# Kernel optimization log

Hardware: AMD Instinct MI355X
Metric: run time of the kernel (lower is better)

## Reference

```python
import jax, jax.numpy as jnp
import numpy as np

B, T, DIN, DH, DE, C = 32, 256, 768, 512, 25, 9


def _xavier(k, shape):
    lim = float(np.sqrt(6.0 / (shape[0] + shape[1])))
    return jax.random.uniform(k, shape, jnp.float32, -lim, lim)


def _unif(k, shape, s):
    return jax.random.uniform(k, shape, jnp.float32, -s, s)


def setup_inputs() -> dict:
    key = jax.random.key(0)
    ks = jax.random.split(key, 14)
    s = 1.0 / float(np.sqrt(DH))
    return {
        "X": jax.random.normal(ks[0], (B, T, DIN), jnp.float32),
        "pad": _xavier(ks[1], (1, DIN)),
        "label_emb": _xavier(ks[2], (C + 1, DE)),
        "Wih_f": _unif(ks[3], (3 * DH, 3 * DIN), s),
        "Whh_f": _unif(ks[4], (3 * DH, DH), s),
        "bih_f": _unif(ks[5], (3 * DH,), s),
        "bhh_f": _unif(ks[6], (3 * DH,), s),
        "Wih_b": _unif(ks[7], (3 * DH, 3 * DIN), s),
        "Whh_b": _unif(ks[8], (3 * DH, DH), s),
        "bih_b": _unif(ks[9], (3 * DH,), s),
        "bhh_b": _unif(ks[10], (3 * DH,), s),
        "Wc": _unif(ks[11], (C, 2 * DH + DE), 1.0 / float(np.sqrt(2 * DH + DE))),
        "bc": _unif(ks[12], (C,), 1.0 / float(np.sqrt(2 * DH + DE))),
    }


def _gru_dir(x, Wih, Whh, bih, bhh, reverse):
    # x: [B, T, 3*DIN]; torch GRU gate order r, z, n
    def step(h, xt):
        gi = xt @ Wih.T + bih              # [B, 3H]
        gh = h @ Whh.T + bhh               # [B, 3H]
        ir, iz, i_n = jnp.split(gi, 3, axis=1)
        hr, hz, h_n = jnp.split(gh, 3, axis=1)
        r = jax.nn.sigmoid(ir + hr)
        z = jax.nn.sigmoid(iz + hz)
        n = jnp.tanh(i_n + r * h_n)
        h = (1.0 - z) * n + z * h
        return h, h
    h0 = jnp.zeros((x.shape[0], Whh.shape[1]), x.dtype)
    _, ys = jax.lax.scan(step, h0, jnp.swapaxes(x, 0, 1), reverse=reverse)
    return jnp.swapaxes(ys, 0, 1)          # [B, T, H]


def reference(X, pad, label_emb, Wih_f, Whh_f, bih_f, bhh_f, Wih_b, Whh_b, bih_b, bhh_b, Wc, bc):
    b = X.shape[0]
    pad_b = jnp.broadcast_to(pad[None, :, :], (b, 1, X.shape[2]))
    X_pad = jnp.concatenate([pad_b, X, pad_b], axis=1)       # [B, T+2, DIN]
    lmr = jnp.concatenate([X_pad[:, :-2, :], X_pad[:, 1:-1, :], X_pad[:, 2:, :]], axis=2)  # [B, T, 3*DIN]
    out_f = _gru_dir(lmr, Wih_f, Whh_f, bih_f, bhh_f, False)
    out_b = _gru_dir(lmr, Wih_b, Whh_b, bih_b, bhh_b, True)
    output_h = jnp.concatenate([out_f, out_b], axis=2)       # [B, T, 2*DH]

    n_labels = label_emb.shape[0] - 1  # start token = last row

    def dec_step(prev, ht):
        # prev: [B] int32 label indices; ht: [B, 2*DH]
        hi = jnp.concatenate([ht, label_emb[prev]], axis=1)   # [B, 2*DH + DE]
        logits = hi @ Wc.T + bc
        probs = jax.nn.softmax(logits, axis=1)
        return jnp.argmax(logits, axis=1).astype(jnp.int32), probs

    prev0 = jnp.full((b,), n_labels, dtype=jnp.int32)
    _, probs_t = jax.lax.scan(dec_step, prev0, jnp.swapaxes(output_h, 0, 1))  # [T, B, C]
    output_chunk = jnp.swapaxes(probs_t, 0, 1).reshape(-1, Wc.shape[0])       # [B*T, C]
    return output_h, output_chunk
```

## Files before the change

kernel.cpp:

```cpp
#include <hip/hip_runtime.h>
#include <hip/hip_bf16.h>
#include <math.h>

#define Bn   32
#define Tn   256
#define DIN  768
#define DHn  512
#define DEn  25
#define Cn   9
#define K3   2304
#define H3   1536
#define NCOL 3072
#define MROW 8192

typedef __attribute__((ext_vector_type(8))) short short8v;
typedef __attribute__((ext_vector_type(4))) float f32x4;

__device__ __forceinline__ unsigned short f2bf(float v) {
  __hip_bfloat16 h = __float2bfloat16(v);
  return __builtin_bit_cast(unsigned short, h);
}
__device__ __forceinline__ float bf2f(unsigned short u) {
  return __bfloat162float(__builtin_bit_cast(__hip_bfloat16, u));
}

#define GBM 128
#define GBN 128
#define GBK 64
#define ASTR 72

__global__ __launch_bounds__(256) void gi_gemm_mfma_kernel(
    const float* __restrict__ X, const float* __restrict__ pad,
    const float* __restrict__ Wf, const float* __restrict__ Wb,
    const float* __restrict__ bf, const float* __restrict__ bb,
    float* __restrict__ gi)
{
  __shared__ __align__(16) unsigned short Ah[GBM * ASTR];
  __shared__ __align__(16) unsigned short Al[GBM * ASTR];
  __shared__ __align__(16) unsigned short Bh[GBN * ASTR];
  __shared__ __align__(16) unsigned short Bl[GBN * ASTR];

  const int bnb = blockIdx.x;
  const int bmb = blockIdx.y;
  const int tid = threadIdx.x;
  const int m0 = bmb * GBM, n0 = bnb * GBN;
  const bool isF = (n0 < H3);
  const float* Wmat = isF ? Wf : Wb;
  const float* bias = isF ? bf : bb;
  const int nb0 = isF ? n0 : (n0 - H3);

  const int r = tid >> 1, half = tid & 1;
  const int m = m0 + r;
  const int ab = m >> 8, tpos = m & 255;
  const float* wrowp = Wmat + (size_t)(nb0 + r) * K3;

  const int wave = tid >> 6, lane = tid & 63;
  const int wr = wave >> 1, wc = wave & 1;
  const int lrow = lane & 15, lk = (lane >> 4) * 8;

  f32x4 acc[4][4];
#pragma unroll
  for (int i = 0; i < 4; i++)
#pragma unroll
    for (int j = 0; j < 4; j++) acc[i][j] = (f32x4){0.f, 0.f, 0.f, 0.f};

  for (int k0 = 0; k0 < K3; k0 += GBK) {
#pragma unroll
    for (int j2 = 0; j2 < 4; j2++) {
      const int kg = k0 + half * 32 + j2 * 8;
      const int seg = (kg >= DIN) + (kg >= 2 * DIN);
      const int off = kg - seg * DIN;
      const int p = tpos + seg;
      const float* srcA = (p == 0 || p == Tn + 1)
                            ? (pad + off)
                            : (X + (size_t)(ab * Tn + (p - 1)) * DIN + off);
      float4 a0 = *reinterpret_cast<const float4*>(srcA);
      float4 a1 = *reinterpret_cast<const float4*>(srcA + 4);
      const float* srcB = wrowp + kg;
      float4 b0 = *reinterpret_cast<const float4*>(srcB);
      float4 b1 = *reinterpret_cast<const float4*>(srcB + 4);

      float av[8] = {a0.x, a0.y, a0.z, a0.w, a1.x, a1.y, a1.z, a1.w};
      float bv[8] = {b0.x, b0.y, b0.z, b0.w, b1.x, b1.y, b1.z, b1.w};
      short8v ah8, al8, bh8, bl8;
#pragma unroll
      for (int q = 0; q < 8; q++) {
        unsigned short h = f2bf(av[q]);
        ah8[q] = (short)h;
        al8[q] = (short)f2bf(av[q] - bf2f(h));
        unsigned short g = f2bf(bv[q]);
        bh8[q] = (short)g;
        bl8[q] = (short)f2bf(bv[q] - bf2f(g));
      }
      const int si = r * ASTR + half * 32 + j2 * 8;
      *reinterpret_cast<short8v*>(&Ah[si]) = ah8;
      *reinterpret_cast<short8v*>(&Al[si]) = al8;
      *reinterpret_cast<short8v*>(&Bh[si]) = bh8;
      *reinterpret_cast<short8v*>(&Bl[si]) = bl8;
    }
    __syncthreads();

#pragma unroll
    for (int ksub = 0; ksub < 2; ksub++) {
      short8v fah[4], fal[4], fbh[4], fbl[4];
#pragma unroll
      for (int i = 0; i < 4; i++) {
        const int ai = (wr * 64 + i * 16 + lrow) * ASTR + ksub * 32 + lk;
        const int bi = (wc * 64 + i * 16 + lrow) * ASTR + ksub * 32 + lk;
        fah[i] = *reinterpret_cast<const short8v*>(&Ah[ai]);
        fal[i] = *reinterpret_cast<const short8v*>(&Al[ai]);
        fbh[i] = *reinterpret_cast<const short8v*>(&Bh[bi]);
        fbl[i] = *reinterpret_cast<const short8v*>(&Bl[bi]);
      }
#pragma unroll
      for (int mi = 0; mi < 4; mi++)
#pragma unroll
        for (int ni = 0; ni < 4; ni++) {
          acc[mi][ni] = __builtin_amdgcn_mfma_f32_16x16x32_bf16(fah[mi], fbh[ni], acc[mi][ni], 0, 0, 0);
          acc[mi][ni] = __builtin_amdgcn_mfma_f32_16x16x32_bf16(fah[mi], fbl[ni], acc[mi][ni], 0, 0, 0);
          acc[mi][ni] = __builtin_amdgcn_mfma_f32_16x16x32_bf16(fal[mi], fbh[ni], acc[mi][ni], 0, 0, 0);
        }
    }
    __syncthreads();
  }

#pragma unroll
  for (int ni = 0; ni < 4; ni++) {
    const int nl = wc * 64 + ni * 16 + (lane & 15);
    const float bvv = bias[nb0 + nl];
#pragma unroll
    for (int mi = 0; mi < 4; mi++) {
      const int mg = m0 + wr * 64 + mi * 16 + (lane >> 4) * 4;
#pragma unroll
      for (int reg = 0; reg < 4; reg++)
        gi[(size_t)(mg + reg) * NCOL + n0 + nl] = acc[mi][ni][reg] + bvv;
    }
  }
}

__global__ __launch_bounds__(256) void prep_kernel(
    const float* __restrict__ Whh_f, const float* __restrict__ Whh_b,
    float4* __restrict__ Wp, unsigned* __restrict__ sync)
{
  int f = blockIdx.x * 256 + threadIdx.x;
  if (f < 8) sync[f * 32] = 0u;
  if (f >= 2 * 32 * 16 * 512) return;
  int k   = f & 511;
  int u   = (f >> 9) & 15;
  int slc = (f >> 13) & 31;
  int d   = f >> 18;
  const float* Wsrc = d ? Whh_b : Whh_f;
  int ug = slc * 16 + u;
  float4 v;
  v.x = Wsrc[(size_t)(0 * DHn + ug) * DHn + k];
  v.y = Wsrc[(size_t)(1 * DHn + ug) * DHn + k];
  v.z = Wsrc[(size_t)(2 * DHn + ug) * DHn + k];
  v.w = 0.f;
  Wp[f] = v;
}

__global__ __launch_bounds__(128) void etab_kernel(
    const float* __restrict__ label_emb, const float* __restrict__ Wc,
    float* __restrict__ etab)
{
  int t = threadIdx.x;
  if (t >= 90) return;
  int p = t / Cn, c = t % Cn;
  float a = 0.f;
#pragma unroll
  for (int j = 0; j < DEn; j++)
    a = fmaf(label_emb[p * DEn + j], Wc[(size_t)c * 1049 + 1024 + j], a);
  etab[t] = a;
}

#define HSTRIDE 12

__global__ __launch_bounds__(512) void gru_rec5_kernel(
    const float* __restrict__ gi,
    const float4* __restrict__ Wp,
    const float* __restrict__ bhh_f, const float* __restrict__ bhh_b,
    unsigned* __restrict__ sync,
    float* __restrict__ hex,
    float* __restrict__ out)
{
  __shared__ __align__(16) float4 Wl[16 * 512];
  __shared__ __align__(16) float hl[512 * HSTRIDE];

  const int bid = blockIdx.x;
  const int xcd = bid & 7;
  const int d = xcd >> 2, g = xcd & 3;
  const int sl = bid >> 3;
  const int tid = threadIdx.x;
  const int ut = tid >> 5;
  const int kq2 = tid & 31;
  const int kq = kq2 & 15, bh = kq2 >> 4;
  const int grp = d * 4 + g;

  {
    const float4* src = Wp + (size_t)(d * 32 + sl) * 8192;
    for (int i = tid; i < 8192; i += 512) Wl[i] = src[i];
  }
  for (int i = tid; i < 512 * HSTRIDE; i += 512) hl[i] = 0.f;

  const float* bhh = d ? bhh_b : bhh_f;
  const int ug = sl * 16 + ut;
  const float br = bhh[ug], bz = bhh[DHn + ug], bn2 = bhh[2 * DHn + ug];
  const int blocal = ((kq & 1) << 1) | ((kq >> 1) & 1);
  const int b_l = bh * 4 + blocal;

  unsigned* cnt = sync + grp * 32;

  __syncthreads();

  for (int s = 0; s < Tn; s++) {
    const int t = d ? (Tn - 1 - s) : s;

    float ir = 0.f, iz = 0.f, inn = 0.f;
    if (kq < 4) {
      const int bg = g * 8 + b_l;
      const float* gp = gi + (size_t)(bg * Tn + t) * NCOL + d * H3 + ug;
      ir = gp[0]; iz = gp[DHn]; inn = gp[2 * DHn];
    }

    if (s > 0) {
      if (tid == 0) {
        const unsigned tgt = 32u * (unsigned)s;
        while (__hip_atomic_load(cnt, __ATOMIC_RELAXED, __HIP_MEMORY_SCOPE_SYSTEM) < tgt)
          __builtin_amdgcn_s_sleep(1);
      }
      __syncthreads();
      asm volatile("" ::: "memory");
      const uint64_t* src = reinterpret_cast<const uint64_t*>(
          hex + (size_t)(((s - 1) & 1) * 8 + grp) * (512 * 8));
#pragma unroll
      for (int j = 0; j < 4; j++) {
        int idx = tid + 512 * j;
        uint64_t v = __hip_atomic_load(src + idx,
                                       __ATOMIC_RELAXED, __HIP_MEMORY_SCOPE_SYSTEM);
        int fd = 2 * idx;
        int u = fd >> 3, b = fd & 7;
        *reinterpret_cast<uint64_t*>(&hl[u * HSTRIDE + b]) = v;
      }
      __syncthreads();
    }

    float acc[3][4];
#pragma unroll
    for (int gg = 0; gg < 3; gg++)
#pragma unroll
      for (int bb = 0; bb < 4; bb++) acc[gg][bb] = 0.f;

#pragma unroll 4
    for (int i = 0; i < 32; i++) {
      int k = i * 16 + kq;
      float4 wv = Wl[ut * 512 + k];
      float4 ha = *reinterpret_cast<const float4*>(&hl[k * HSTRIDE + bh * 4]);
      acc[0][0] = fmaf(wv.x, ha.x, acc[0][0]); acc[0][1] = fmaf(wv.x, ha.y, acc[0][1]);
      acc[0][2] = fmaf(wv.x, ha.z, acc[0][2]); acc[0][3] = fmaf(wv.x, ha.w, acc[0][3]);
      acc[1][0] = fmaf(wv.y, ha.x, acc[1][0]); acc[1][1] = fmaf(wv.y, ha.y, acc[1][1]);
      acc[1][2] = fmaf(wv.y, ha.z, acc[1][2]); acc[1][3] = fmaf(wv.y, ha.w, acc[1][3]);
      acc[2][0] = fmaf(wv.z, ha.x, acc[2][0]); acc[2][1] = fmaf(wv.z, ha.y, acc[2][1]);
      acc[2][2] = fmaf(wv.z, ha.z, acc[2][2]); acc[2][3] = fmaf(wv.z, ha.w, acc[2][3]);
    }

#pragma unroll
    for (int gg = 0; gg < 3; gg++)
#pragma unroll
      for (int bb = 0; bb < 4; bb++)
        acc[gg][bb] += __shfl_xor(acc[gg][bb], 8);

    float a2[3][2];
#pragma unroll
    for (int gg = 0; gg < 3; gg++)
#pragma unroll
      for (int j = 0; j < 2; j++) {
        float keep = (kq & 1) ? acc[gg][2 + j] : acc[gg][j];
        float send = (kq & 1) ? acc[gg][j] : acc[gg][2 + j];
        a2[gg][j] = keep + __shfl_xor(send, 1);
      }
    float a1[3];
#pragma unroll
    for (int gg = 0; gg < 3; gg++) {
      float keep = (kq & 2) ? a2[gg][1] : a2[gg][0];
      float send = (kq & 2) ? a2[gg][0] : a2[gg][1];
      a1[gg] = keep + __shfl_xor(send, 2);
    }
#pragma unroll
    for (int gg = 0; gg < 3; gg++)
      a1[gg] += __shfl_xor(a1[gg], 4);

    float hnew = 0.f;
    if (kq < 4) {
      const float r = 1.f / (1.f + expf(-(ir + a1[0] + br)));
      const float z = 1.f / (1.f + expf(-(iz + a1[1] + bz)));
      const float n = tanhf(inn + r * (a1[2] + bn2));
      const float hold = hl[ug * HSTRIDE + b_l];
      hnew = (1.f - z) * n + z * hold;
      __hip_atomic_store(&hex[((size_t)(s & 1) * 8 + grp) * (512 * 8) + ug * 8 + b_l],
                         hnew, __ATOMIC_RELAXED, __HIP_MEMORY_SCOPE_SYSTEM);
    }
    __syncthreads();
    if (s < Tn - 1 && tid == 0)
      __hip_atomic_fetch_add(cnt, 1u, __ATOMIC_RELAXED, __HIP_MEMORY_SCOPE_SYSTEM);
    if (kq < 4)
      out[(size_t)((g * 8 + b_l) * Tn + t) * 1024 + d * DHn + ug] = hnew;
  }
}

__global__ __launch_bounds__(256) void lh_kernel(
    const float* __restrict__ out_h, const float* __restrict__ Wc,
    const float* __restrict__ bc, float* __restrict__ lh)
{
  const int tid = threadIdx.x;
  const int wave = tid >> 6, lane = tid & 63;
#pragma unroll 1
  for (int it = 0; it < 16; it++) {
    const int row = blockIdx.x * 64 + wave * 16 + it;
    const float* hp = out_h + (size_t)row * 1024 + lane * 4;
    float4 hv[4];
#pragma unroll
    for (int j = 0; j < 4; j++) hv[j] = *reinterpret_cast<const float4*>(hp + 256 * j);
    float acc[Cn];
#pragma unroll
    for (int c = 0; c < Cn; c++) {
      const float* wp = Wc + (size_t)c * 1049 + lane * 4;
      float a = 0.f;
#pragma unroll
      for (int j = 0; j < 4; j++) {
        float4 wv = *reinterpret_cast<const float4*>(wp + 256 * j);
        a = fmaf(hv[j].x, wv.x, a); a = fmaf(hv[j].y, wv.y, a);
        a = fmaf(hv[j].z, wv.z, a); a = fmaf(hv[j].w, wv.w, a);
      }
      acc[c] = a;
    }
#pragma unroll
    for (int off = 32; off; off >>= 1)
#pragma unroll
      for (int c = 0; c < Cn; c++) acc[c] += __shfl_xor(acc[c], off);
    if (lane < Cn) lh[(size_t)row * 12 + lane] = acc[lane] + bc[lane];
  }
}

__global__ __launch_bounds__(64) void chain_kernel(
    const float* __restrict__ lh,
    const float* __restrict__ etab,
    float* __restrict__ outc)
{
  __shared__ float et[90];
  const int tid = threadIdx.x;
  if (tid < 90) et[tid] = etab[tid];
  __syncthreads();
  if (tid >= Bn) return;
  const int b = tid;
  const float* base = lh + (size_t)b * Tn * 12;
  float4 A0 = *reinterpret_cast<const float4*>(base);
  float4 A1 = *reinterpret_cast<const float4*>(base + 4);
  float c8 = base[8];
  int prev = Cn;
  for (int t = 0; t < Tn; t++) {
    float4 N0 = {0,0,0,0}, N1 = {0,0,0,0}; float nc8 = 0.f;
    if (t < Tn - 1) {
      const float* nb = base + (size_t)(t + 1) * 12;
      N0 = *reinterpret_cast<const float4*>(nb);
      N1 = *reinterpret_cast<const float4*>(nb + 4);
      nc8 = nb[8];
    }
    float lg[Cn] = {A0.x, A0.y, A0.z, A0.w, A1.x, A1.y, A1.z, A1.w, c8};
    const float* ep = &et[prev * Cn];
#pragma unroll
    for (int c = 0; c < Cn; c++) lg[c] += ep[c];
    float mx = lg[0]; int idx = 0;
#pragma unroll
    for (int c = 1; c < Cn; c++) if (lg[c] > mx) { mx = lg[c]; idx = c; }
    float e[Cn]; float sum = 0.f;
#pragma unroll
    for (int c = 0; c < Cn; c++) { e[c] = expf(lg[c] - mx); sum += e[c]; }
    const float inv = 1.f / sum;
    float* op = outc + ((size_t)b * Tn + t) * Cn;
#pragma unroll
    for (int c = 0; c < Cn; c++) op[c] = e[c] * inv;
    prev = idx;
    A0 = N0; A1 = N1; c8 = nc8;
  }
}

extern "C" void kernel_launch(void* const* d_in, const int* in_sizes, int n_in,
                              void* d_out, int out_size, void* d_ws, size_t ws_size,
                              hipStream_t stream) {
  const float* X      = (const float*)d_in[0];
  const float* pad    = (const float*)d_in[1];
  const float* lemb   = (const float*)d_in[2];
  const float* Wih_f  = (const float*)d_in[3];
  const float* Whh_f  = (const float*)d_in[4];
  const float* bih_f  = (const float*)d_in[5];
  const float* bhh_f  = (const float*)d_in[6];
  const float* Wih_b  = (const float*)d_in[7];
  const float* Whh_b  = (const float*)d_in[8];
  const float* bih_b  = (const float*)d_in[9];
  const float* bhh_b  = (const float*)d_in[10];
  const float* Wc     = (const float*)d_in[11];
  const float* bc     = (const float*)d_in[12];
  float* out = (float*)d_out;

  char* ws = (char*)d_ws;
  float*    gi   = (float*)ws;
  float4*   Wp   = (float4*)(ws + (size_t)MROW * NCOL * 4);
  unsigned* sync = (unsigned*)(ws + (size_t)MROW * NCOL * 4 + 8388608);
  float*    hex  = (float*)(ws + (size_t)MROW * NCOL * 4 + 8388608 + 1024);
  float*    lh   = (float*)ws;
  float*    etab = (float*)(ws + 524288);

  prep_kernel<<<dim3(2048), dim3(256), 0, stream>>>(Whh_f, Whh_b, Wp, sync);
  gi_gemm_mfma_kernel<<<dim3(NCOL / GBN, MROW / GBM), dim3(256), 0, stream>>>(
      X, pad, Wih_f, Wih_b, bih_f, bih_b, gi);
  gru_rec5_kernel<<<dim3(256), dim3(512), 0, stream>>>(gi, Wp, bhh_f, bhh_b, sync, hex, out);
  etab_kernel<<<dim3(1), dim3(128), 0, stream>>>(lemb, Wc, etab);
  lh_kernel<<<dim3(128), dim3(256), 0, stream>>>(out, Wc, bc, lh);
  chain_kernel<<<dim3(1), dim3(64), 0, stream>>>(lh, etab, out + (size_t)MROW * 1024);
}
```

Measured before the change: 1.918 ms.

## Pre-convert GEMM operands to split bf16 and use per-wave barrier arrivals in GRU

Adds kernels that convert X (with padding rows) and Wih once into hi/lo bf16 arrays, so the input-projection GEMM loads bf16 tiles instead of re-splitting fp32 in every tile. This path runs only when the workspace is large enough. The GRU recurrence now has every thread spin on the cross-block counter, and each wave increments it after a vmcnt wait, replacing the tid-0 spin plus two block barriers per step. This shortens the critical path of the serial recurrence, at the cost of more atomic polling traffic and extra workspace and conversion passes.

```diff
diff --git a/kernel.cpp b/kernel.cpp
--- a/kernel.cpp
+++ b/kernel.cpp
@@ -24,10 +24,152 @@
   return __bfloat162float(__builtin_bit_cast(__hip_bfloat16, u));
 }
 
+__global__ __launch_bounds__(256) void prep_x_kernel(
+    const float* __restrict__ X, const float* __restrict__ pad,
+    unsigned short* __restrict__ Xh, unsigned short* __restrict__ Xl)
+{
+  int e = blockIdx.x * 256 + threadIdx.x;
+  if (e >= 32 * 258 * 96) return;
+  int k8 = e % 96;
+  int row = e / 96;
+  int p = row % 258, b = row / 258;
+  int off = k8 * 8;
+  const float* src = (p == 0 || p == 257) ? (pad + off)
+                                          : (X + (size_t)(b * Tn + (p - 1)) * DIN + off);
+  float4 v0 = *reinterpret_cast<const float4*>(src);
+  float4 v1 = *reinterpret_cast<const float4*>(src + 4);
+  float av[8] = {v0.x, v0.y, v0.z, v0.w, v1.x, v1.y, v1.z, v1.w};
+  short8v h8, l8;
+#pragma unroll
+  for (int q = 0; q < 8; q++) {
+    unsigned short h = f2bf(av[q]);
+    h8[q] = (short)h;
+    l8[q] = (short)f2bf(av[q] - bf2f(h));
+  }
+  *reinterpret_cast<short8v*>(Xh + (size_t)row * DIN + off) = h8;
+  *reinterpret_cast<short8v*>(Xl + (size_t)row * DIN + off) = l8;
+}
+
+__global__ __launch_bounds__(256) void prep_wih_kernel(
+    const float* __restrict__ Wf, const float* __restrict__ Wb,
+    unsigned short* __restrict__ Bh, unsigned short* __restrict__ Bl)
+{
+  int e = blockIdx.x * 256 + threadIdx.x;
+  if (e >= 3072 * 288) return;
+  int k8 = e % 288;
+  int rr = e / 288;
+  int off = k8 * 8;
+  const float* src = (rr < H3) ? (Wf + (size_t)rr * K3 + off)
+                               : (Wb + (size_t)(rr - H3) * K3 + off);
+  float4 v0 = *reinterpret_cast<const float4*>(src);
+  float4 v1 = *reinterpret_cast<const float4*>(src + 4);
+  float av[8] = {v0.x, v0.y, v0.z, v0.w, v1.x, v1.y, v1.z, v1.w};
+  short8v h8, l8;
+#pragma unroll
+  for (int q = 0; q < 8; q++) {
+    unsigned short h = f2bf(av[q]);
+    h8[q] = (short)h;
+    l8[q] = (short)f2bf(av[q] - bf2f(h));
+  }
+  *reinterpret_cast<short8v*>(Bh + (size_t)rr * K3 + off) = h8;
+  *reinterpret_cast<short8v*>(Bl + (size_t)rr * K3 + off) = l8;
+}
+
 #define GBM 128
 #define GBN 128
 #define GBK 64
 #define ASTR 72
+
+__global__ __launch_bounds__(256) void gi_gemm_pc_kernel(
+    const unsigned short* __restrict__ Xh, const unsigned short* __restrict__ Xl,
+    const unsigned short* __restrict__ Bh, const unsigned short* __restrict__ Bl,
+    const float* __restrict__ bf, const float* __restrict__ bb,
+    float* __restrict__ gi)
+{
+  __shared__ __align__(16) unsigned short LAh[GBM * ASTR];
+  __shared__ __align__(16) unsigned short LAl[GBM * ASTR];
+  __shared__ __align__(16) unsigned short LBh[GBN * ASTR];
+  __shared__ __align__(16) unsigned short LBl[GBN * ASTR];
+
+  const int bnb = blockIdx.x, bmb = blockIdx.y;
+  const int tid = threadIdx.x;
+  const int m0 = bmb * GBM, n0 = bnb * GBN;
+  const bool isF = (n0 < H3);
+  const float* bias = isF ? bf : bb;
+  const int nb0 = isF ? n0 : (n0 - H3);
+
+  const int r = tid >> 1, half = tid & 1;
+  const int m = m0 + r;
+  const int ab = m >> 8, tpos = m & 255;
+
+  const int wave = tid >> 6, lane = tid & 63;
+  const int wr = wave >> 1, wc = wave & 1;
+  const int lrow = lane & 15, lk = (lane >> 4) * 8;
+
+  f32x4 acc[4][4];
+#pragma unroll
+  for (int i = 0; i < 4; i++)
+#pragma unroll
+    for (int j = 0; j < 4; j++) acc[i][j] = (f32x4){0.f, 0.f, 0.f, 0.f};
+
+  for (int k0 = 0; k0 < K3; k0 += GBK) {
+#pragma unroll
+    for (int j2 = 0; j2 < 4; j2++) {
+      const int kg = k0 + half * 32 + j2 * 8;
+      const int seg = (kg >= DIN) + (kg >= 2 * DIN);
+      const int off = kg - seg * DIN;
+      const int p = tpos + seg;
+      const size_t xi = (size_t)(ab * 258 + p) * DIN + off;
+      const size_t bi = (size_t)(n0 + r) * K3 + kg;
+      short8v a_h = *reinterpret_cast<const short8v*>(Xh + xi);
+      short8v a_l = *reinterpret_cast<const short8v*>(Xl + xi);
+      short8v b_h = *reinterpret_cast<const short8v*>(Bh + bi);
+      short8v b_l = *reinterpret_cast<const short8v*>(Bl + bi);
+      const int si = r * ASTR + half * 32 + j2 * 8;
+      *reinterpret_cast<short8v*>(&LAh[si]) = a_h;
+      *reinterpret_cast<short8v*>(&LAl[si]) = a_l;
+      *reinterpret_cast<short8v*>(&LBh[si]) = b_h;
+      *reinterpret_cast<short8v*>(&LBl[si]) = b_l;
+    }
+    __syncthreads();
+
+#pragma unroll
+    for (int ksub = 0; ksub < 2; ksub++) {
+      short8v fah[4], fal[4], fbh[4], fbl[4];
+#pragma unroll
+      for (int i = 0; i < 4; i++) {
+        const int ai = (wr * 64 + i * 16 + lrow) * ASTR + ksub * 32 + lk;
+        const int bi2 = (wc * 64 + i * 16 + lrow) * ASTR + ksub * 32 + lk;
+        fah[i] = *reinterpret_cast<const short8v*>(&LAh[ai]);
+        fal[i] = *reinterpret_cast<const short8v*>(&LAl[ai]);
+        fbh[i] = *reinterpret_cast<const short8v*>(&LBh[bi2]);
+        fbl[i] = *reinterpret_cast<const short8v*>(&LBl[bi2]);
+      }
+#pragma unroll
+      for (int mi = 0; mi < 4; mi++)
+#pragma unroll
+        for (int ni = 0; ni < 4; ni++) {
+          acc[mi][ni] = __builtin_amdgcn_mfma_f32_16x16x32_bf16(fah[mi], fbh[ni], acc[mi][ni], 0, 0, 0);
+          acc[mi][ni] = __builtin_amdgcn_mfma_f32_16x16x32_bf16(fah[mi], fbl[ni], acc[mi][ni], 0, 0, 0);
+          acc[mi][ni] = __builtin_amdgcn_mfma_f32_16x16x32_bf16(fal[mi], fbh[ni], acc[mi][ni], 0, 0, 0);
+        }
+    }
+    __syncthreads();
+  }
+
+#pragma unroll
+  for (int ni = 0; ni < 4; ni++) {
+    const int nl = wc * 64 + ni * 16 + (lane & 15);
+    const float bvv = bias[nb0 + nl];
+#pragma unroll
+    for (int mi = 0; mi < 4; mi++) {
+      const int mg = m0 + wr * 64 + mi * 16 + (lane >> 4) * 4;
+#pragma unroll
+      for (int reg = 0; reg < 4; reg++)
+        gi[(size_t)(mg + reg) * NCOL + n0 + nl] = acc[mi][ni][reg] + bvv;
+    }
+  }
+}
 
 __global__ __launch_bounds__(256) void gi_gemm_mfma_kernel(
     const float* __restrict__ X, const float* __restrict__ pad,
@@ -37,11 +179,10 @@
 {
   __shared__ __align__(16) unsigned short Ah[GBM * ASTR];
   __shared__ __align__(16) unsigned short Al[GBM * ASTR];
-  __shared__ __align__(16) unsigned short Bh[GBN * ASTR];
-  __shared__ __align__(16) unsigned short Bl[GBN * ASTR];
-
-  const int bnb = blockIdx.x;
-  const int bmb = blockIdx.y;
+  __shared__ __align__(16) unsigned short Bh2[GBN * ASTR];
+  __shared__ __align__(16) unsigned short Bl2[GBN * ASTR];
+
+  const int bnb = blockIdx.x, bmb = blockIdx.y;
   const int tid = threadIdx.x;
   const int m0 = bmb * GBM, n0 = bnb * GBN;
   const bool isF = (n0 < H3);
@@ -79,7 +220,6 @@
       const float* srcB = wrowp + kg;
       float4 b0 = *reinterpret_cast<const float4*>(srcB);
       float4 b1 = *reinterpret_cast<const float4*>(srcB + 4);
-
       float av[8] = {a0.x, a0.y, a0.z, a0.w, a1.x, a1.y, a1.z, a1.w};
       float bv[8] = {b0.x, b0.y, b0.z, b0.w, b1.x, b1.y, b1.z, b1.w};
       short8v ah8, al8, bh8, bl8;
@@ -95,11 +235,10 @@
       const int si = r * ASTR + half * 32 + j2 * 8;
       *reinterpret_cast<short8v*>(&Ah[si]) = ah8;
       *reinterpret_cast<short8v*>(&Al[si]) = al8;
-      *reinterpret_cast<short8v*>(&Bh[si]) = bh8;
-      *reinterpret_cast<short8v*>(&Bl[si]) = bl8;
+      *reinterpret_cast<short8v*>(&Bh2[si]) = bh8;
+      *reinterpret_cast<short8v*>(&Bl2[si]) = bl8;
     }
     __syncthreads();
-
 #pragma unroll
     for (int ksub = 0; ksub < 2; ksub++) {
       short8v fah[4], fal[4], fbh[4], fbl[4];
@@ -109,8 +248,8 @@
         const int bi = (wc * 64 + i * 16 + lrow) * ASTR + ksub * 32 + lk;
         fah[i] = *reinterpret_cast<const short8v*>(&Ah[ai]);
         fal[i] = *reinterpret_cast<const short8v*>(&Al[ai]);
-        fbh[i] = *reinterpret_cast<const short8v*>(&Bh[bi]);
-        fbl[i] = *reinterpret_cast<const short8v*>(&Bl[bi]);
+        fbh[i] = *reinterpret_cast<const short8v*>(&Bh2[bi]);
+        fbl[i] = *reinterpret_cast<const short8v*>(&Bl2[bi]);
       }
 #pragma unroll
       for (int mi = 0; mi < 4; mi++)
@@ -123,7 +262,6 @@
     }
     __syncthreads();
   }
-
 #pragma unroll
   for (int ni = 0; ni < 4; ni++) {
     const int nl = wc * 64 + ni * 16 + (lane & 15);
@@ -175,7 +313,7 @@
 
 #define HSTRIDE 12
 
-__global__ __launch_bounds__(512) void gru_rec5_kernel(
+__global__ __launch_bounds__(512) void gru_rec6_kernel(
     const float* __restrict__ gi,
     const float4* __restrict__ Wp,
     const float* __restrict__ bhh_f, const float* __restrict__ bhh_b,
@@ -223,12 +361,9 @@
     }
 
     if (s > 0) {
-      if (tid == 0) {
-        const unsigned tgt = 32u * (unsigned)s;
-        while (__hip_atomic_load(cnt, __ATOMIC_RELAXED, __HIP_MEMORY_SCOPE_SYSTEM) < tgt)
-          __builtin_amdgcn_s_sleep(1);
-      }
-      __syncthreads();
+      const unsigned tgt = 256u * (unsigned)s;
+      while (__hip_atomic_load(cnt, __ATOMIC_RELAXED, __HIP_MEMORY_SCOPE_SYSTEM) < tgt)
+        __builtin_amdgcn_s_sleep(1);
       asm volatile("" ::: "memory");
       const uint64_t* src = reinterpret_cast<const uint64_t*>(
           hex + (size_t)(((s - 1) & 1) * 8 + grp) * (512 * 8));
@@ -241,8 +376,8 @@
         int u = fd >> 3, b = fd & 7;
         *reinterpret_cast<uint64_t*>(&hl[u * HSTRIDE + b]) = v;
       }
-      __syncthreads();
-    }
+    }
+    __syncthreads();
 
     float acc[3][4];
 #pragma unroll
@@ -289,21 +424,19 @@
     for (int gg = 0; gg < 3; gg++)
       a1[gg] += __shfl_xor(a1[gg], 4);
 
-    float hnew = 0.f;
     if (kq < 4) {
       const float r = 1.f / (1.f + expf(-(ir + a1[0] + br)));
       const float z = 1.f / (1.f + expf(-(iz + a1[1] + bz)));
       const float n = tanhf(inn + r * (a1[2] + bn2));
       const float hold = hl[ug * HSTRIDE + b_l];
-      hnew = (1.f - z) * n + z * hold;
+      const float hnew = (1.f - z) * n + z * hold;
       __hip_atomic_store(&hex[((size_t)(s & 1) * 8 + grp) * (512 * 8) + ug * 8 + b_l],
                          hnew, __ATOMIC_RELAXED, __HIP_MEMORY_SCOPE_SYSTEM);
-    }
-    __syncthreads();
-    if (s < Tn - 1 && tid == 0)
+      out[(size_t)((g * 8 + b_l) * Tn + t) * 1024 + d * DHn + ug] = hnew;
+    }
+    asm volatile("s_waitcnt vmcnt(0)" ::: "memory");
+    if (s < Tn - 1 && (tid & 63) == 0)
       __hip_atomic_fetch_add(cnt, 1u, __ATOMIC_RELAXED, __HIP_MEMORY_SCOPE_SYSTEM);
-    if (kq < 4)
-      out[(size_t)((g * 8 + b_l) * Tn + t) * 1024 + d * DHn + ug] = hnew;
   }
 }
 
@@ -342,8 +475,7 @@
 }
 
 __global__ __launch_bounds__(64) void chain_kernel(
-    const float* __restrict__ lh,
-    const float* __restrict__ etab,
+    const float* __restrict__ lh, const float* __restrict__ etab,
     float* __restrict__ outc)
 {
   __shared__ float et[90];
@@ -404,16 +536,29 @@
 
   char* ws = (char*)d_ws;
   float*    gi   = (float*)ws;
-  float4*   Wp   = (float4*)(ws + (size_t)MROW * NCOL * 4);
-  unsigned* sync = (unsigned*)(ws + (size_t)MROW * NCOL * 4 + 8388608);
-  float*    hex  = (float*)(ws + (size_t)MROW * NCOL * 4 + 8388608 + 1024);
+  float4*   Wp   = (float4*)(ws + 100663296);
+  unsigned* sync = (unsigned*)(ws + 109051904);
+  float*    hex  = (float*)(ws + 109052928);
+  unsigned short* Xh = (unsigned short*)(ws + 109315072);
+  unsigned short* Xl = (unsigned short*)(ws + 121996288);
+  unsigned short* Bh = (unsigned short*)(ws + 134677504);
+  unsigned short* Bl = (unsigned short*)(ws + 148833280);
   float*    lh   = (float*)ws;
   float*    etab = (float*)(ws + 524288);
 
+  const bool preconv = (ws_size >= (size_t)162989056ULL);
+
   prep_kernel<<<dim3(2048), dim3(256), 0, stream>>>(Whh_f, Whh_b, Wp, sync);
-  gi_gemm_mfma_kernel<<<dim3(NCOL / GBN, MROW / GBM), dim3(256), 0, stream>>>(
-      X, pad, Wih_f, Wih_b, bih_f, bih_b, gi);
-  gru_rec5_kernel<<<dim3(256), dim3(512), 0, stream>>>(gi, Wp, bhh_f, bhh_b, sync, hex, out);
+  if (preconv) {
+    prep_x_kernel<<<dim3((32 * 258 * 96 + 255) / 256), dim3(256), 0, stream>>>(X, pad, Xh, Xl);
+    prep_wih_kernel<<<dim3((3072 * 288 + 255) / 256), dim3(256), 0, stream>>>(Wih_f, Wih_b, Bh, Bl);
+    gi_gemm_pc_kernel<<<dim3(NCOL / GBN, MROW / GBM), dim3(256), 0, stream>>>(
+        Xh, Xl, Bh, Bl, bih_f, bih_b, gi);
+  } else {
+    gi_gemm_mfma_kernel<<<dim3(NCOL / GBN, MROW / GBM), dim3(256), 0, stream>>>(
+        X, pad, Wih_f, Wih_b, bih_f, bih_b, gi);
+  }
+  gru_rec6_kernel<<<dim3(256), dim3(512), 0, stream>>>(gi, Wp, bhh_f, bhh_b, sync, hex, out);
   etab_kernel<<<dim3(1), dim3(128), 0, stream>>>(lemb, Wc, etab);
   lh_kernel<<<dim3(128), dim3(256), 0, stream>>>(out, Wc, bc, lh);
   chain_kernel<<<dim3(1), dim3(64), 0, stream>>>(lh, etab, out + (size_t)MROW * 1024);
```

Result: slower. 3.492 ms (+82.1%).
